# Performance work log

Hardware: AMD Instinct MI355X
Metric: run time of the kernel (lower is better)

The kernel has to match this reference:

```python
import jax, jax.numpy as jnp
import numpy as np

TEMPERATURE = 0.5
EPS = 1e-8  # torch F.cosine_similarity denominator clamp


def setup_inputs() -> dict:
    key = jax.random.key(0)
    k1, k2 = jax.random.split(key)
    B, D = 4096, 128
    return {
        "z_i": jax.random.normal(k1, (B, D), dtype=jnp.float32),
        "z_j": jax.random.normal(k2, (B, D), dtype=jnp.float32),
    }


def reference(z_i, z_j):
    B = z_i.shape[0]
    n2 = 2 * B
    reps = jnp.concatenate([z_i, z_j], axis=0)  # [2B, D]
    norms = jnp.maximum(jnp.linalg.norm(reps, axis=1, keepdims=True), EPS)
    rn = reps / norms
    # full pairwise cosine similarity matrix [2B, 2B]
    sim = rn @ rn.T
    # positives: sim[i, i+B] and sim[i+B, i]
    pos = jnp.concatenate([jnp.diagonal(sim, offset=B), jnp.diagonal(sim, offset=-B)])  # [2B]
    # Cross-entropy with label 0 on logits [pos, negatives]/T is equivalent to
    # -pos/T + logsumexp over {pos} U {negatives} = logsumexp over all j != i.
    diag_mask = jnp.eye(n2, dtype=bool)
    logits = jnp.where(diag_mask, -jnp.inf, sim / TEMPERATURE)
    lse = jax.nn.logsumexp(logits, axis=1)  # [2B]
    loss = jnp.sum(lse - pos / TEMPERATURE) / n2
    return loss
```

## Files before the change

kernel.cpp:

```cpp
#include <hip/hip_runtime.h>
#include <hip/hip_bf16.h>

#define B_ROWS 4096
#define N2     8192
#define DIM    128
#define LN2    0.6931471805599453f
#define S_SCALE 1.6986436f

typedef __attribute__((ext_vector_type(8))) short bf16x8;
typedef __attribute__((ext_vector_type(4))) float f32x4;

#if __has_builtin(__builtin_amdgcn_exp2f)
#define EXP2F(x) __builtin_amdgcn_exp2f(x)
#else
#define EXP2F(x) __expf((x) * LN2)
#endif
#if __has_builtin(__builtin_amdgcn_logf)
#define LOG2F_FAST(x) __builtin_amdgcn_logf(x)
#else
#define LOG2F_FAST(x) log2f(x)
#endif

static __device__ __forceinline__ unsigned short f2bf(float f) {
    union { float f; unsigned int u; } v; v.f = f;
    unsigned int u = v.u;
    return (unsigned short)((u + 0x7fffu + ((u >> 16) & 1u)) >> 16);
}
static __device__ __forceinline__ float bf2f(unsigned short s) {
    union { unsigned int u; float f; } v; v.u = ((unsigned int)s) << 16;
    return v.f;
}
static __device__ __forceinline__ void gload_lds16(const void* g, void* l) {
    __builtin_amdgcn_global_load_lds(
        (const __attribute__((address_space(1))) void*)g,
        (__attribute__((address_space(3))) void*)l, 16, 0, 0);
}

__global__ __launch_bounds__(256) void nk_normalize(
        const float* __restrict__ zi, const float* __restrict__ zj,
        unsigned short* __restrict__ rn, float* __restrict__ selfexp,
        float* __restrict__ out) {
    int gtid = blockIdx.x * 256 + threadIdx.x;
    if (gtid == 0) out[0] = 0.0f;
    int row  = gtid >> 6;
    int lane = threadIdx.x & 63;
    const float* src = (row < B_ROWS) ? (zi + (size_t)row * DIM)
                                      : (zj + (size_t)(row - B_ROWS) * DIM);
    float2 v = reinterpret_cast<const float2*>(src)[lane];
    float ss = v.x * v.x + v.y * v.y;
#pragma unroll
    for (int m = 1; m < 64; m <<= 1) ss += __shfl_xor(ss, m);
    float scale = S_SCALE / fmaxf(sqrtf(ss), 1e-8f);
    ushort2 o;
    o.x = f2bf(v.x * scale);
    o.y = f2bf(v.y * scale);
    reinterpret_cast<ushort2*>(rn + (size_t)row * DIM)[lane] = o;
    float a = bf2f(o.x), b = bf2f(o.y);
    float sd = a * a + b * b;
#pragma unroll
    for (int m = 1; m < 64; m <<= 1) sd += __shfl_xor(sd, m);
    if (lane == 0) selfexp[row] = EXP2F(sd);
}

__global__ __launch_bounds__(256, 4) void nk_simloss(
        const unsigned short* __restrict__ rn, float* __restrict__ part_out) {
    __shared__ char lds[2][16384];
    const int tid = threadIdx.x;
    const int bi = blockIdx.x >> 4;
    const int bc = blockIdx.x & 15;
    const int w = tid >> 6, lane = tid & 63;
    const int lc = lane & 15, lg = lane >> 4;
    const int i0 = bi * 128 + w * 32;

    const unsigned short* abase = rn + (size_t)(i0 + lc) * DIM + lg * 8;
    bf16x8 af[2][4];
#pragma unroll
    for (int mi = 0; mi < 2; ++mi)
#pragma unroll
        for (int ks = 0; ks < 4; ++ks)
            af[mi][ks] = *reinterpret_cast<const bf16x8*>(
                abase + (size_t)mi * 16 * DIM + ks * 32);

    const char* gsrc = (const char*)rn + (size_t)bc * 512 * 256;

#define STAGE(b, t)                                                           \
    do {                                                                      \
        _Pragma("unroll") for (int k = 0; k < 4; ++k) {                       \
            int L  = k * 4096 + tid * 16;                                     \
            int Ls = L ^ (((L >> 8) & 7) << 4);                               \
            gload_lds16(gsrc + (size_t)(t) * 16384 + Ls,                      \
                        &lds[b][k * 4096 + (tid & 192) * 16]);                \
        }                                                                     \
    } while (0)

    float part[2][4];
#pragma unroll
    for (int mi = 0; mi < 2; ++mi)
#pragma unroll
        for (int p = 0; p < 4; ++p) part[mi][p] = 0.f;

    STAGE(0, 0);
    __syncthreads();

#pragma unroll 1
    for (int t = 0; t < 8; ++t) {
        const int cur = t & 1;
        if (t < 7) STAGE(cur ^ 1, t + 1);
        const char* tb = lds[cur];
#pragma unroll
        for (int s = 0; s < 4; ++s) {
            bf16x8 bf[4];
#pragma unroll
            for (int ks = 0; ks < 4; ++ks) {
                int r = s * 16 + lc;
                int a = r * 256 + ks * 64 + lg * 16;
                a ^= (r & 7) << 4;
                bf[ks] = *reinterpret_cast<const bf16x8*>(tb + a);
            }
            f32x4 acc[2];
#pragma unroll
            for (int mi = 0; mi < 2; ++mi) acc[mi] = (f32x4){0.f, 0.f, 0.f, 0.f};
#pragma unroll
            for (int ks = 0; ks < 4; ++ks)
#pragma unroll
                for (int mi = 0; mi < 2; ++mi)
                    acc[mi] = __builtin_amdgcn_mfma_f32_16x16x32_bf16(
                        af[mi][ks], bf[ks], acc[mi], 0, 0, 0);
#pragma unroll
            for (int mi = 0; mi < 2; ++mi)
#pragma unroll
                for (int p = 0; p < 4; ++p)
                    part[mi][p] += EXP2F(acc[mi][p]);
        }
        __syncthreads();
    }
#undef STAGE

#pragma unroll
    for (int mi = 0; mi < 2; ++mi)
#pragma unroll
        for (int p = 0; p < 4; ++p) {
            float v = part[mi][p];
#pragma unroll
            for (int m = 1; m < 16; m <<= 1) v += __shfl_xor(v, m);
            if (lc == 0)
                part_out[(size_t)bc * N2 + i0 + mi * 16 + lg * 4 + p] = v;
        }
}

__global__ __launch_bounds__(256) void nk_finalize(
        const unsigned short* __restrict__ rn, const float* __restrict__ part,
        const float* __restrict__ selfexp, float* __restrict__ out) {
    int wid = threadIdx.x >> 6, lane = threadIdx.x & 63;
    int lc = lane & 15, lg = lane >> 4;
    int wavegid = blockIdx.x * 4 + wid;
    float acc = 0.f;
    for (int base = wavegid * 4; base < N2; base += 512 * 4) {
        int row = base + lg;
        bf16x8 a = *reinterpret_cast<const bf16x8*>(rn + (size_t)row * DIM + lc * 8);
        bf16x8 b = *reinterpret_cast<const bf16x8*>(rn + (size_t)(row ^ B_ROWS) * DIM + lc * 8);
        float d = 0.f;
#pragma unroll
        for (int e = 0; e < 8; ++e)
            d += bf2f((unsigned short)a[e]) * bf2f((unsigned short)b[e]);
        float rs = part[(size_t)lc * N2 + row];
#pragma unroll
        for (int m = 1; m < 16; m <<= 1) {
            d  += __shfl_xor(d, m);
            rs += __shfl_xor(rs, m);
        }
        if (lc == 0)
            acc += LOG2F_FAST(rs - selfexp[row]) - d;
    }
#pragma unroll
    for (int m = 1; m < 64; m <<= 1) acc += __shfl_xor(acc, m);
    if (lane == 0) atomicAdd(out, acc * (LN2 / (float)N2));
}

extern "C" void kernel_launch(void* const* d_in, const int* in_sizes, int n_in,
                              void* d_out, int out_size, void* d_ws, size_t ws_size,
                              hipStream_t stream) {
    const float* zi = (const float*)d_in[0];
    const float* zj = (const float*)d_in[1];
    float* out = (float*)d_out;

    unsigned short* rn = (unsigned short*)d_ws;
    float* part    = (float*)((char*)d_ws + (size_t)N2 * DIM * 2);
    float* selfexp = part + 16 * N2;

    nk_normalize<<<2048, 256, 0, stream>>>(zi, zj, rn, selfexp, out);
    nk_simloss<<<1024, 256, 0, stream>>>(rn, part);
    nk_finalize<<<128, 256, 0, stream>>>(rn, part, selfexp, out);
}
```

Baseline: 91.22 us.

## Fuse finalize into simloss via atomic row sums and last-block reduction

Drops the separate finalize kernel. Each simloss block now atomically adds its partial row sums into a single rowsum array instead of writing 16 separate partial slices, and also computes the positive-pair dot products for 8 rows. The last block to finish, detected with an atomic counter, performs the log-sum and the final reduction. This removes one kernel launch and the partial-sum traffic, at the cost of float atomics contending on row sums and a serial tail run by one block.

```diff
diff --git a/kernel.cpp b/kernel.cpp
--- a/kernel.cpp
+++ b/kernel.cpp
@@ -39,9 +39,10 @@
 __global__ __launch_bounds__(256) void nk_normalize(
         const float* __restrict__ zi, const float* __restrict__ zj,
         unsigned short* __restrict__ rn, float* __restrict__ selfexp,
-        float* __restrict__ out) {
+        float* __restrict__ rowsum, int* __restrict__ done) {
     int gtid = blockIdx.x * 256 + threadIdx.x;
-    if (gtid == 0) out[0] = 0.0f;
+    if (gtid < N2) rowsum[gtid] = 0.0f;
+    if (gtid == 0) *done = 0;
     int row  = gtid >> 6;
     int lane = threadIdx.x & 63;
     const float* src = (row < B_ROWS) ? (zi + (size_t)row * DIM)
@@ -63,7 +64,9 @@
 }
 
 __global__ __launch_bounds__(256, 4) void nk_simloss(
-        const unsigned short* __restrict__ rn, float* __restrict__ part_out) {
+        const unsigned short* __restrict__ rn, float* __restrict__ rowsum,
+        const float* __restrict__ selfexp, float* __restrict__ posv,
+        int* __restrict__ done, float* __restrict__ out) {
     __shared__ char lds[2][16384];
     const int tid = threadIdx.x;
     const int bi = blockIdx.x >> 4;
@@ -144,37 +147,43 @@
 #pragma unroll
             for (int m = 1; m < 16; m <<= 1) v += __shfl_xor(v, m);
             if (lc == 0)
-                part_out[(size_t)bc * N2 + i0 + mi * 16 + lg * 4 + p] = v;
+                atomicAdd(&rowsum[i0 + mi * 16 + lg * 4 + p], v);
         }
-}
-
-__global__ __launch_bounds__(256) void nk_finalize(
-        const unsigned short* __restrict__ rn, const float* __restrict__ part,
-        const float* __restrict__ selfexp, float* __restrict__ out) {
-    int wid = threadIdx.x >> 6, lane = threadIdx.x & 63;
-    int lc = lane & 15, lg = lane >> 4;
-    int wavegid = blockIdx.x * 4 + wid;
+
+    {
+        int prow = blockIdx.x * 8 + (tid >> 5);
+        int sub  = tid & 31;
+        const unsigned short* pa = rn + (size_t)prow * DIM + sub * 4;
+        const unsigned short* pb = rn + (size_t)(prow ^ B_ROWS) * DIM + sub * 4;
+        uint2 va = *reinterpret_cast<const uint2*>(pa);
+        uint2 vb = *reinterpret_cast<const uint2*>(pb);
+        float d = bf2f((unsigned short)(va.x & 0xffff)) * bf2f((unsigned short)(vb.x & 0xffff))
+                + bf2f((unsigned short)(va.x >> 16))    * bf2f((unsigned short)(vb.x >> 16))
+                + bf2f((unsigned short)(va.y & 0xffff)) * bf2f((unsigned short)(vb.y & 0xffff))
+                + bf2f((unsigned short)(va.y >> 16))    * bf2f((unsigned short)(vb.y >> 16));
+#pragma unroll
+        for (int m = 1; m < 32; m <<= 1) d += __shfl_xor(d, m);
+        if (sub == 0) posv[prow] = d;
+    }
+
+    __threadfence();
+    __syncthreads();
+    __shared__ int lastflag;
+    if (tid == 0) lastflag = (atomicAdd(done, 1) == 1023);
+    __syncthreads();
+    if (!lastflag) return;
+    __threadfence();
     float acc = 0.f;
-    for (int base = wavegid * 4; base < N2; base += 512 * 4) {
-        int row = base + lg;
-        bf16x8 a = *reinterpret_cast<const bf16x8*>(rn + (size_t)row * DIM + lc * 8);
-        bf16x8 b = *reinterpret_cast<const bf16x8*>(rn + (size_t)(row ^ B_ROWS) * DIM + lc * 8);
-        float d = 0.f;
-#pragma unroll
-        for (int e = 0; e < 8; ++e)
-            d += bf2f((unsigned short)a[e]) * bf2f((unsigned short)b[e]);
-        float rs = part[(size_t)lc * N2 + row];
-#pragma unroll
-        for (int m = 1; m < 16; m <<= 1) {
-            d  += __shfl_xor(d, m);
-            rs += __shfl_xor(rs, m);
-        }
-        if (lc == 0)
-            acc += LOG2F_FAST(rs - selfexp[row]) - d;
+    for (int r = tid; r < N2; r += 256)
+        acc += LOG2F_FAST(rowsum[r] - selfexp[r]) - posv[r];
+    float* red = (float*)lds;
+    red[tid] = acc;
+    __syncthreads();
+    for (int off = 128; off > 0; off >>= 1) {
+        if (tid < off) red[tid] += red[tid + off];
+        __syncthreads();
     }
-#pragma unroll
-    for (int m = 1; m < 64; m <<= 1) acc += __shfl_xor(acc, m);
-    if (lane == 0) atomicAdd(out, acc * (LN2 / (float)N2));
+    if (tid == 0) out[0] = red[0] * (LN2 / (float)N2);
 }
 
 extern "C" void kernel_launch(void* const* d_in, const int* in_sizes, int n_in,
@@ -185,10 +194,11 @@
     float* out = (float*)d_out;
 
     unsigned short* rn = (unsigned short*)d_ws;
-    float* part    = (float*)((char*)d_ws + (size_t)N2 * DIM * 2);
-    float* selfexp = part + 16 * N2;
-
-    nk_normalize<<<2048, 256, 0, stream>>>(zi, zj, rn, selfexp, out);
-    nk_simloss<<<1024, 256, 0, stream>>>(rn, part);
-    nk_finalize<<<128, 256, 0, stream>>>(rn, part, selfexp, out);
-}
+    float* rowsum  = (float*)((char*)d_ws + (size_t)N2 * DIM * 2);
+    float* selfexp = rowsum + N2;
+    float* posv    = selfexp + N2;
+    int*   done    = (int*)(posv + N2);
+
+    nk_normalize<<<2048, 256, 0, stream>>>(zi, zj, rn, selfexp, rowsum, done);
+    nk_simloss<<<1024, 256, 0, stream>>>(rn, rowsum, selfexp, posv, done, out);
+}
```

Result: slower. 148.1 us (+62.3%).
